# Kernel tuning notes

Hardware: AMD Instinct MI355X
Metric: run time of the kernel (lower is better)

## Reference

```python
import jax, jax.numpy as jnp
import numpy as np

HIDDEN = 512
B, H, W = 8, 48, 48
SCALE = 1.0 / np.sqrt(HIDDEN).astype(np.float32)


def conv1x1(x, w, b):
    # x: [B, C, H, W], w: [O, C], b: [O]  (1x1 Conv2d == channel matmul)
    return jnp.einsum('bchw,oc->bohw', x, w) + b[None, :, None, None]


def setup_inputs() -> dict:
    key = jax.random.key(0)
    ks = jax.random.split(key, 10)
    s = 1.0 / np.sqrt(HIDDEN)
    return {
        'locx': jax.random.normal(ks[0], (B, HIDDEN, H, W), dtype=jnp.float32),
        'glox': jax.random.normal(ks[1], (B, HIDDEN, H, W), dtype=jnp.float32),
        'Wq': jax.random.normal(ks[2], (HIDDEN, HIDDEN), dtype=jnp.float32) * s,
        'bq': jax.random.normal(ks[3], (HIDDEN,), dtype=jnp.float32) * 0.01,
        'Wk': jax.random.normal(ks[4], (HIDDEN, HIDDEN), dtype=jnp.float32) * s,
        'bk': jax.random.normal(ks[5], (HIDDEN,), dtype=jnp.float32) * 0.01,
        'Wv': jax.random.normal(ks[6], (HIDDEN, HIDDEN), dtype=jnp.float32) * s,
        'bv': jax.random.normal(ks[7], (HIDDEN,), dtype=jnp.float32) * 0.01,
        'Wo': jax.random.normal(ks[8], (HIDDEN, HIDDEN), dtype=jnp.float32) * s,
        'bo': jax.random.normal(ks[9], (HIDDEN,), dtype=jnp.float32) * 0.01,
    }


def reference(locx, glox, Wq, bq, Wk, bk, Wv, bv, Wo, bo):
    b, c, h, w = locx.shape
    # 1x1 conv projections
    q = conv1x1(locx, Wq, bq).reshape(b, c, h * w)   # [B, C, N]
    k = conv1x1(glox, Wk, bk).reshape(b, c, -1)      # [B, C, M]
    v = conv1x1(glox, Wv, bv).reshape(b, c, -1)      # [B, C, M]
    # scores = Q^T K / sqrt(hidden)  -> [B, N, M]
    scores = jnp.einsum('bcn,bcm->bnm', q, k) * SCALE
    probs = jax.nn.softmax(scores, axis=-1)           # dropout rate 0.0 -> identity
    # context = probs @ V^T -> [B, N, C] -> [B, C, H, H]
    ctx = jnp.einsum('bnm,bcm->bcn', probs, v).reshape(b, c, h, h)
    out = conv1x1(ctx, Wo, bo)                        # proj dropout 0.0 -> identity
    return out
```

## Files before the change

### kernel.cpp

```cpp
#include <hip/hip_runtime.h>
#include <hip/hip_bf16.h>

typedef __attribute__((ext_vector_type(4))) float f32x4;
typedef __attribute__((ext_vector_type(8))) short bf16x8;
typedef __attribute__((ext_vector_type(4))) short s16x4;

#define C_DIM 512
#define N_PIX 2304
#define N_BATCH 8
#define ATT_SCALE 0.04419417382415922f
#define NJB 9

typedef __attribute__((address_space(3))) unsigned int lds_u32;
typedef const __attribute__((address_space(1))) unsigned int glob_u32;

__device__ __forceinline__ void gl2lds16(const __hip_bfloat16* g, __hip_bfloat16* l)
{
    __builtin_amdgcn_global_load_lds((glob_u32*)g, (lds_u32*)l, 16, 0, 0);
}

#define GBAR() __builtin_amdgcn_s_barrier()
#define GVM0() asm volatile("s_waitcnt vmcnt(0)" ::: "memory")


#define BAR()  __builtin_amdgcn_s_barrier()
#define LGK0() asm volatile("s_waitcnt lgkmcnt(0)" ::: "memory")
#define VM4()  asm volatile("s_waitcnt vmcnt(4)" ::: "memory")
#define VM0()  asm volatile("s_waitcnt vmcnt(0)" ::: "memory")
#define PRIO(p) __builtin_amdgcn_s_setprio(p)

#define STAGE_A(dd, hh, tk) do { \
    _Pragma("unroll") \
    for (int ss = 0; ss < 2; ++ss) { \
        const int ur0 = wave * 16 + ss * 8; \
        const int row0 = ((ur0 >> 6) << 7) + (hh) * 64 + (ur0 & 63); \
        gl2lds16(gA + (size_t)row0 * C_DIM + (tk) * 64, \
                 (__hip_bfloat16*)&LA[dd][row0 * 64]); \
    } } while (0)

#define STAGE_B(dd, bb, tk) do { \
    _Pragma("unroll") \
    for (int ss = 0; ss < 2; ++ss) { \
        const int ur0 = wave * 16 + ss * 8; \
        const int row0 = ((ur0 >> 5) << 6) + (bb) * 32 + (ur0 & 31); \
        gl2lds16(gB + (size_t)row0 * C_DIM + (tk) * 64, \
                 (__hip_bfloat16*)&LB[dd][row0 * 64]); \
    } } while (0)

#define LOAD_A(dd, hh) do { \
    _Pragma("unroll") \
    for (int tt = 0; tt < 4; ++tt) { \
        const int rb = (wr * 128 + (hh) * 64 + tt * 16 + fr) * 64; \
        _Pragma("unroll") \
        for (int kk = 0; kk < 2; ++kk) \
            aF[tt][kk] = *(const bf16x8*)(&LA[dd][rb + (((kk * 4 + fq) ^ sw) << 3)]); \
    } } while (0)

#define LOAD_B(dd, bb, dst) do { \
    _Pragma("unroll") \
    for (int s2 = 0; s2 < 2; ++s2) { \
        const int rb = (wc * 64 + (bb) * 32 + s2 * 16 + fr) * 64; \
        _Pragma("unroll") \
        for (int kk = 0; kk < 2; ++kk) \
            dst[s2][kk] = *(const bf16x8*)(&LB[dd][rb + (((kk * 4 + fq) ^ sw) << 3)]); \
    } } while (0)

#define MFMA_Q(HH, BB, bsrc) do { \
    _Pragma("unroll") \
    for (int tt = 0; tt < 4; ++tt) \
    _Pragma("unroll") \
    for (int s2 = 0; s2 < 2; ++s2) \
    _Pragma("unroll") \
    for (int kk = 0; kk < 2; ++kk) \
        acc[(HH) * 4 + tt][(BB) * 2 + s2] = __builtin_amdgcn_mfma_f32_16x16x32_bf16( \
            aF[tt][kk], bsrc[s2][kk], acc[(HH) * 4 + tt][(BB) * 2 + s2], 0, 0, 0); \
    } while (0)

template<int NS>
__global__ __launch_bounds__(512, 2)
void s_vp(const __hip_bfloat16* __restrict__ Qt, const __hip_bfloat16* __restrict__ Kt,
          __hip_bfloat16* __restrict__ Pu, float* __restrict__ rp,
          const __hip_bfloat16* __restrict__ wo, const __hip_bfloat16* __restrict__ Vt,
          __hip_bfloat16* __restrict__ Vp, int bz_off, long sPu)
{
    __shared__ __hip_bfloat16 LA[2][256 * 64];
    __shared__ __hip_bfloat16 LB[2][256 * 64];

    const int lin = blockIdx.x;
    const int bz  = lin % NS + bz_off;
    const int t   = lin / NS;
    const bool is_s = (t < 81);

    int ib, jb;
    const __hip_bfloat16 *A, *B;
    __hip_bfloat16* D;
    const long sQ = (long)N_PIX * C_DIM;
    if (is_s) {
        ib = t / 9; jb = t % 9;
        A = Qt + (size_t)bz * sQ;
        B = Kt + (size_t)bz * sQ;
        D = Pu + (size_t)bz * (size_t)sPu;
    } else {
        int u = t - 81;
        ib = u / 9; jb = u % 9;
        A = wo;
        B = Vt + (size_t)bz * sQ;
        D = Vp + (size_t)bz * sQ;
    }
    const int i0 = ib * 256;
    const int j0 = jb * 256;

    const int tid  = threadIdx.x;
    const int lane = tid & 63;
    const int wave = tid >> 6;

    const int lrow = lane >> 3;
    const int lcs  = (lane & 7) ^ lrow;
    const __hip_bfloat16* gA = A + (size_t)(i0 + lrow) * C_DIM + lcs * 8;
    const __hip_bfloat16* gB = B + (size_t)(j0 + lrow) * C_DIM + lcs * 8;

    const int fr = lane & 15;
    const int fq = lane >> 4;
    const int sw = fr & 7;
    const int wr = wave >> 2;
    const int wc = wave & 3;

    f32x4 acc[8][4];
#pragma unroll
    for (int a = 0; a < 8; ++a)
#pragma unroll
        for (int b = 0; b < 4; ++b)
            acc[a][b] = (f32x4){0.f, 0.f, 0.f, 0.f};

    bf16x8 aF[4][2], bF0[2][2], bF1[2][2];

    STAGE_A(0, 0, 0); STAGE_B(0, 0, 0); STAGE_B(0, 1, 0); STAGE_A(0, 1, 0);
    STAGE_A(1, 0, 1); STAGE_B(1, 1, 1);
    VM4();
    BAR();

    for (int kt = 0; kt < 6; ++kt) {
        const int d = kt & 1, e = d ^ 1;
        LOAD_A(d, 0); LOAD_B(d, 0, bF0);
        STAGE_A(e, 1, kt + 1);
        BAR(); LGK0();
        PRIO(1); MFMA_Q(0, 0, bF0); PRIO(0);
        BAR();
        LOAD_B(d, 1, bF1);
        STAGE_B(e, 0, kt + 1);
        BAR(); LGK0();
        PRIO(1); MFMA_Q(0, 1, bF1); PRIO(0);
        BAR();
        LOAD_A(d, 1);
        STAGE_A(d, 0, kt + 2);
        BAR(); LGK0();
        PRIO(1); MFMA_Q(1, 1, bF1); PRIO(0);
        BAR();
        STAGE_B(d, 1, kt + 2);
        VM4();
        BAR();
        PRIO(1); MFMA_Q(1, 0, bF0); PRIO(0);
        BAR();
    }
    {
        LOAD_A(0, 0); LOAD_B(0, 0, bF0);
        STAGE_A(1, 1, 7);
        BAR(); LGK0();
        PRIO(1); MFMA_Q(0, 0, bF0); PRIO(0);
        BAR();
        LOAD_B(0, 1, bF1);
        STAGE_B(1, 0, 7);
        BAR(); LGK0();
        PRIO(1); MFMA_Q(0, 1, bF1); PRIO(0);
        BAR();
        LOAD_A(0, 1);
        BAR(); LGK0();
        PRIO(1); MFMA_Q(1, 1, bF1); PRIO(0);
        BAR();
        VM0();
        BAR();
        PRIO(1); MFMA_Q(1, 0, bF0); PRIO(0);
        BAR();
    }
    {
        LOAD_A(1, 0); LOAD_B(1, 0, bF0);
        BAR(); LGK0();
        PRIO(1); MFMA_Q(0, 0, bF0); PRIO(0);
        BAR();
        LOAD_B(1, 1, bF1);
        BAR(); LGK0();
        PRIO(1); MFMA_Q(0, 1, bF1); PRIO(0);
        BAR();
        LOAD_A(1, 1);
        BAR(); LGK0();
        PRIO(1); MFMA_Q(1, 1, bF1); PRIO(0);
        BAR();
        PRIO(1); MFMA_Q(1, 0, bF0); PRIO(0);
    }

    if (is_s) {
        float rpart[8][4];
#pragma unroll
        for (int a = 0; a < 8; ++a)
#pragma unroll
            for (int r = 0; r < 4; ++r)
                rpart[a][r] = 0.f;
#pragma unroll
        for (int a = 0; a < 8; ++a) {
            const int grow = i0 + wr * 128 + a * 16 + fq * 4;
#pragma unroll
            for (int b = 0; b < 4; ++b) {
                const int col = j0 + wc * 64 + b * 16 + fr;
#pragma unroll
                for (int r = 0; r < 4; ++r) {
                    float v = __expf(acc[a][b][r] * ATT_SCALE);
                    rpart[a][r] += v;
                    D[(size_t)(grow + r) * N_PIX + col] = __float2bfloat16(v);
                }
            }
        }
#pragma unroll
        for (int m = 1; m < 16; m <<= 1)
#pragma unroll
            for (int a = 0; a < 8; ++a)
#pragma unroll
                for (int r = 0; r < 4; ++r)
                    rpart[a][r] += __shfl_xor(rpart[a][r], m);
        float* rsl = (float*)&LA[0][0];
        __syncthreads();
        if (fr == 0) {
#pragma unroll
            for (int a = 0; a < 8; ++a)
#pragma unroll
                for (int r = 0; r < 4; ++r)
                    rsl[wave * 128 + a * 16 + fq * 4 + r] = rpart[a][r];
        }
        __syncthreads();
        if (tid < 256) {
            const int wr2 = tid >> 7, rl = tid & 127;
            float s = rsl[(wr2 * 4 + 0) * 128 + rl] + rsl[(wr2 * 4 + 1) * 128 + rl]
                    + rsl[(wr2 * 4 + 2) * 128 + rl] + rsl[(wr2 * 4 + 3) * 128 + rl];
            rp[((size_t)jb * N_BATCH + bz) * N_PIX + i0 + tid] = s;
        }
    } else {
#pragma unroll
        for (int a = 0; a < 8; ++a) {
            const int grow = i0 + wr * 128 + a * 16 + fq * 4;
#pragma unroll
            for (int b = 0; b < 4; ++b) {
                const int col = j0 + wc * 64 + b * 16 + fr;
#pragma unroll
                for (int r = 0; r < 4; ++r)
                    D[(size_t)(grow + r) * N_PIX + col] = __float2bfloat16(acc[a][b][r]);
            }
        }
    }
}

#undef STAGE_A
#undef STAGE_B
#undef LOAD_A
#undef LOAD_B
#undef MFMA_Q
#undef BAR
#undef LGK0
#undef VM4
#undef VM0
#undef PRIO


#define PV_STAGE(ee, tk) do { \
    _Pragma("unroll") \
    for (int ss = 0; ss < 2; ++ss) \
        gl2lds16(ga + (size_t)ss * 8 * N_PIX + (tk) * 64, \
                 laA + (ee) * (64 * 64) + ss * 8 * 64); \
    _Pragma("unroll") \
    for (int ss = 0; ss < 4; ++ss) \
        gl2lds16(gb + (size_t)ss * 8 * N_PIX + (tk) * 64, \
                 laB + (ee) * (128 * 64) + ss * 8 * 64); \
    } while (0)

#define PV_COMP(dd) do { \
    _Pragma("unroll") \
    for (int kk = 0; kk < 2; ++kk) { \
        bf16x8 af[2], bfr[4]; \
        const int ca = ((kk * 4 + fq) ^ sw) << 3; \
        _Pragma("unroll") \
        for (int tt = 0; tt < 2; ++tt) \
            af[tt]  = *(const bf16x8*)(&As[dd][(wi + tt * 16 + fr) * 64 + ca]); \
        _Pragma("unroll") \
        for (int tt = 0; tt < 4; ++tt) \
            bfr[tt] = *(const bf16x8*)(&Bs[dd][(wj + tt * 16 + fr) * 64 + ca]); \
        _Pragma("unroll") \
        for (int a = 0; a < 2; ++a) \
        _Pragma("unroll") \
        for (int b = 0; b < 4; ++b) \
            acc[a][b] = __builtin_amdgcn_mfma_f32_16x16x32_bf16( \
                af[a], bfr[b], acc[a][b], 0, 0, 0); \
    } } while (0)

template<int NS>
__global__ __launch_bounds__(256)
void pv_out(const __hip_bfloat16* __restrict__ Vp, const __hip_bfloat16* __restrict__ Pu,
            float* __restrict__ out, const float* __restrict__ bo,
            const float* __restrict__ rp, int bz_off, long sPu)
{
    __shared__ __hip_bfloat16 As[2][64 * 64];
    __shared__ __hip_bfloat16 Bs[2][128 * 64];

    const int lin = blockIdx.x;
    const int bz  = lin % NS + bz_off;
    const int t   = lin / NS;
    const int ib  = t % 8;
    const int jb  = t / 8;
    const int i0  = ib * 64;
    const int j0  = jb * 128;

    const long sCN = (long)C_DIM * N_PIX;
    const __hip_bfloat16* A = Vp + (size_t)bz * sCN;
    const __hip_bfloat16* B = Pu + (size_t)bz * (size_t)sPu;
    float* D = out + (size_t)bz * sCN;

    const int tid  = threadIdx.x;
    const int lane = tid & 63;
    const int wave = tid >> 6;

    const int lrow = lane >> 3;
    const int lcs  = (lane & 7) ^ lrow;
    const __hip_bfloat16* ga = A + (size_t)(i0 + wave * 16 + lrow) * N_PIX + lcs * 8;
    const __hip_bfloat16* gb = B + (size_t)(j0 + wave * 32 + lrow) * N_PIX + lcs * 8;
    __hip_bfloat16* laA = &As[0][wave * 16 * 64];
    __hip_bfloat16* laB = &Bs[0][wave * 32 * 64];

    const int fr = lane & 15;
    const int fq = lane >> 4;
    const int sw = fr & 7;
    const int wi = (wave >> 1) * 32;
    const int wj = (wave & 1) * 64;

    f32x4 acc[2][4];
#pragma unroll
    for (int a = 0; a < 2; ++a)
#pragma unroll
        for (int b = 0; b < 4; ++b)
            acc[a][b] = (f32x4){0.f, 0.f, 0.f, 0.f};

    PV_STAGE(0, 0);
    GVM0(); GBAR();

#pragma unroll 1
    for (int kt = 0; kt < 34; kt += 2) {
        PV_STAGE(1, kt + 1);
        PV_COMP(0);
        GVM0(); GBAR();
        PV_STAGE(0, kt + 2);
        PV_COMP(1);
        GVM0(); GBAR();
    }
    PV_STAGE(1, 35);
    PV_COMP(0);
    GVM0(); GBAR();
    PV_COMP(1);

    const int orow = fq * 4;
    float rjv[4];
#pragma unroll
    for (int b = 0; b < 4; ++b) {
        int j = j0 + wj + b * 16 + fr;
        float s = 0.f;
#pragma unroll
        for (int jj = 0; jj < NJB; ++jj)
            s += rp[((size_t)jj * N_BATCH + bz) * N_PIX + j];
        rjv[b] = 1.f / s;
    }

#pragma unroll
    for (int a = 0; a < 2; ++a) {
        int ibx = i0 + wi + a * 16 + orow;
#pragma unroll
        for (int r = 0; r < 4; ++r) {
            float bi = bo[ibx + r];
#pragma unroll
            for (int b = 0; b < 4; ++b) {
                int j = j0 + wj + b * 16 + fr;
                D[(size_t)(ibx + r) * N_PIX + j] = acc[a][b][r] * rjv[b] + bi;
            }
        }
    }
}

#undef PV_STAGE
#undef PV_COMP


#define PJ_STAGE(ee, tk) do { \
    _Pragma("unroll") \
    for (int ss = 0; ss < 4; ++ss) { \
        gl2lds16(ga + (size_t)ss * 8 * C_DIM + (tk) * 64, \
                 laA + (ee) * (128 * 64) + ss * 8 * 64); \
        gl2lds16(gb + (size_t)ss * 8 * C_DIM + (tk) * 64, \
                 laB + (ee) * (128 * 64) + ss * 8 * 64); \
    } } while (0)

#define PJ_COMP(dd) do { \
    _Pragma("unroll") \
    for (int kk = 0; kk < 2; ++kk) { \
        bf16x8 af[4], bfr[4]; \
        const int ca = ((kk * 4 + fq) ^ sw) << 3; \
        _Pragma("unroll") \
        for (int tt = 0; tt < 4; ++tt) { \
            af[tt]  = *(const bf16x8*)(&As[dd][(wi + tt * 16 + fr) * 64 + ca]); \
            bfr[tt] = *(const bf16x8*)(&Bs[dd][(wj + tt * 16 + fr) * 64 + ca]); \
        } \
        _Pragma("unroll") \
        for (int a = 0; a < 4; ++a) \
        _Pragma("unroll") \
        for (int b = 0; b < 4; ++b) \
            acc[a][b] = __builtin_amdgcn_mfma_f32_16x16x32_bf16( \
                af[a], bfr[b], acc[a][b], 0, 0, 0); \
    } } while (0)

__global__ __launch_bounds__(256)
void proj_qkv(const __hip_bfloat16* __restrict__ Xl,
              const __hip_bfloat16* __restrict__ Xg,
              const __hip_bfloat16* __restrict__ wgt,
              const float* __restrict__ bq, const float* __restrict__ bk,
              const float* __restrict__ bv,
              __hip_bfloat16* __restrict__ QKV)
{
    __shared__ __hip_bfloat16 As[2][128 * 64];
    __shared__ __hip_bfloat16 Bs[2][128 * 64];

    const int lin = blockIdx.x;
    const int s   = lin % 24;
    const int bz  = s & 7;
    const int mat = s >> 3;
    const int t   = lin / 24;
    const int j0  = (t & 3) * 128;
    const int i0  = (t >> 2) * 128;

    const __hip_bfloat16* Ab = ((mat == 0) ? Xl : Xg) + (size_t)bz * N_PIX * C_DIM;
    const __hip_bfloat16* Bb = wgt + (size_t)mat * C_DIM * C_DIM;
    const float* bias = (mat == 0) ? bq : (mat == 1) ? bk : bv;
    __hip_bfloat16* D = QKV + ((size_t)mat * N_BATCH + bz) * N_PIX * C_DIM;

    const int tid  = threadIdx.x;
    const int lane = tid & 63;
    const int wave = tid >> 6;

    const int lrow = lane >> 3;
    const int lcs  = (lane & 7) ^ lrow;
    const __hip_bfloat16* ga = Ab + (size_t)(i0 + wave * 32 + lrow) * C_DIM + lcs * 8;
    const __hip_bfloat16* gb = Bb + (size_t)(j0 + wave * 32 + lrow) * C_DIM + lcs * 8;
    __hip_bfloat16* laA = &As[0][wave * 32 * 64];
    __hip_bfloat16* laB = &Bs[0][wave * 32 * 64];

    const int fr = lane & 15;
    const int fq = lane >> 4;
    const int sw = fr & 7;
    const int wi = (wave >> 1) * 64;
    const int wj = (wave & 1) * 64;

    f32x4 acc[4][4];
#pragma unroll
    for (int a = 0; a < 4; ++a)
#pragma unroll
        for (int b = 0; b < 4; ++b)
            acc[a][b] = (f32x4){0.f, 0.f, 0.f, 0.f};

    PJ_STAGE(0, 0);
    GVM0(); GBAR();

#pragma unroll 1
    for (int kt = 0; kt < 6; kt += 2) {
        PJ_STAGE(1, kt + 1);
        PJ_COMP(0);
        GVM0(); GBAR();
        PJ_STAGE(0, kt + 2);
        PJ_COMP(1);
        GVM0(); GBAR();
    }
    PJ_STAGE(1, 7);
    PJ_COMP(0);
    GVM0(); GBAR();
    PJ_COMP(1);

    const int orow = fq * 4;
#pragma unroll
    for (int a = 0; a < 4; ++a) {
        int ibx = i0 + wi + a * 16 + orow;
#pragma unroll
        for (int b = 0; b < 4; ++b) {
            int j = j0 + wj + b * 16 + fr;
            float bj = bias[j];
#pragma unroll
            for (int r = 0; r < 4; ++r)
                D[(size_t)(ibx + r) * C_DIM + j] = __float2bfloat16(acc[a][b][r] + bj);
        }
    }
}

#undef PJ_STAGE
#undef PJ_COMP

__global__ __launch_bounds__(256)
void prep(const float* __restrict__ locx, const float* __restrict__ glox,
          __hip_bfloat16* __restrict__ Xl, __hip_bfloat16* __restrict__ Xg,
          const float* __restrict__ w0, const float* __restrict__ w1,
          const float* __restrict__ w2, const float* __restrict__ w3,
          __hip_bfloat16* __restrict__ wgt)
{
    const int lin = blockIdx.x;
    const int tid = threadIdx.x;

    if (lin < 4608) {
        __shared__ float t[64 * 65];
        const int z  = lin & 15;
        const int t2 = lin >> 4;
        const int c0 = (t2 & 7) * 64;
        const int n0 = (t2 >> 3) * 64;
        const size_t b = z & 7;
        const float* Xb = ((z < 8) ? locx : glox) + b * (size_t)C_DIM * N_PIX;
        __hip_bfloat16* Xt = (z < 8) ? Xl : Xg;

        const int n_l = tid & 63;
        const int c_b = tid >> 6;
#pragma unroll
        for (int s = 0; s < 16; ++s) {
            int c_l = c_b + s * 4;
            t[c_l * 65 + n_l] = Xb[(size_t)(c0 + c_l) * N_PIX + n0 + n_l];
        }
        __syncthreads();

        const int cc = (tid & 7) * 8;
        const int nb = tid >> 3;
#pragma unroll
        for (int it = 0; it < 2; ++it) {
            int n2 = nb + it * 32;
            union { __hip_bfloat16 h[8]; int4 v; } u;
#pragma unroll
            for (int w = 0; w < 8; ++w)
                u.h[w] = __float2bfloat16(t[(cc + w) * 65 + n2]);
            *(int4*)(&Xt[(b * N_PIX + n0 + n2) * C_DIM + c0 + cc]) = u.v;
        }
    } else {
        const int idx = lin - 4608;
        const int w   = idx >> 8;
        const float* srcs[4] = {w0, w1, w2, w3};
        const int i = ((idx & 255) * 256 + tid) * 4;
        float4 f = *(const float4*)(srcs[w] + i);
        union { __hip_bfloat16 h[4]; s16x4 q; } u;
        u.h[0] = __float2bfloat16(f.x);
        u.h[1] = __float2bfloat16(f.y);
        u.h[2] = __float2bfloat16(f.z);
        u.h[3] = __float2bfloat16(f.w);
        *(s16x4*)(wgt + (size_t)w * C_DIM * C_DIM + i) = u.q;
    }
}

extern "C" void kernel_launch(void* const* d_in, const int* in_sizes, int n_in,
                              void* d_out, int out_size, void* d_ws, size_t ws_size,
                              hipStream_t stream)
{
    const float* locx = (const float*)d_in[0];
    const float* glox = (const float*)d_in[1];
    const float* Wq = (const float*)d_in[2];
    const float* bq = (const float*)d_in[3];
    const float* Wk = (const float*)d_in[4];
    const float* bk = (const float*)d_in[5];
    const float* Wv = (const float*)d_in[6];
    const float* bv = (const float*)d_in[7];
    const float* Wo = (const float*)d_in[8];
    const float* bo = (const float*)d_in[9];
    float* out = (float*)d_out;

    const int C = C_DIM, N = N_PIX;
    const size_t WB   = (size_t)C * C * 2;
    const size_t szX  = (size_t)N_BATCH * N * C * 2;
    const size_t szP1 = (size_t)N * N * 2;
    const size_t szRP = (size_t)NJB * N_BATCH * N * 4;

    const size_t fixed = 4 * WB + 6 * szX + szRP;
    bool full = (ws_size >= fixed + 8 * szP1 + 4096);

    char* ws = (char*)d_ws;
    size_t off = 0;
    auto alloc = [&](size_t bytes) {
        char* p = ws + off;
        off += (bytes + 255) & ~(size_t)255;
        return p;
    };
    __hip_bfloat16* wgt = (__hip_bfloat16*)alloc(4 * WB);
    __hip_bfloat16* Xl  = (__hip_bfloat16*)alloc(szX);
    __hip_bfloat16* Xg  = (__hip_bfloat16*)alloc(szX);
    __hip_bfloat16* QKV = (__hip_bfloat16*)alloc(3 * szX);
    __hip_bfloat16* Vp  = (__hip_bfloat16*)alloc(szX);
    float*          rp  = (float*)alloc(szRP);
    __hip_bfloat16* Pu  = (__hip_bfloat16*)alloc(full ? 8 * szP1 : szP1);

    __hip_bfloat16* Qt = QKV;
    __hip_bfloat16* Kt = QKV + (size_t)N_BATCH * N * C;
    __hip_bfloat16* Vt = QKV + 2 * (size_t)N_BATCH * N * C;
    __hip_bfloat16* wo_b = wgt + 3 * (size_t)C * C;

    const dim3 blk(256);

    prep<<<dim3(5632), blk, 0, stream>>>(locx, glox, Xl, Xg, Wq, Wk, Wv, Wo, wgt);
    proj_qkv<<<dim3(24 * 72), blk, 0, stream>>>(Xl, Xg, wgt, bq, bk, bv, QKV);

    if (full) {
        s_vp<8><<<dim3(8 * 99), dim3(512), 0, stream>>>(
            Qt, Kt, Pu, rp, wo_b, Vt, Vp, 0, (long)N * N);
        pv_out<8><<<dim3(8 * 144), blk, 0, stream>>>(
            Vp, Pu, out, bo, rp, 0, (long)N * N);
    } else {
        for (int r = 0; r < N_BATCH; ++r) {
            s_vp<1><<<dim3(99), dim3(512), 0, stream>>>(
                Qt, Kt, Pu, rp, wo_b, Vt, Vp, r, 0);
            pv_out<1><<<dim3(144), blk, 0, stream>>>(
                Vp, Pu, out, bo, rp, r, 0);
        }
    }
}
```

Measured before the change: 329.6 us.

## Fold Q/K and V/O weights into combined matrices to drop projection GEMMs

Rewrites the attention algebraically. Scores become Xl·(Wq^T Wk)·Xg^T plus a per-key term Xg·(Wk^T bq); the per-query terms cancel in softmax, which is why bk is dropped. The V and output projections are merged into one Wo·Wv matrix, applied directly to Xg with a folded bias Wo·bv, and written transposed. This removes one full projection GEMM and the separate Wo·V tiles in the score kernel, at the cost of an extra small weight-mixing kernel and more bf16 rounding through the combined weights.

Result: slower. 359.9 us (+9.2%).

```diff
diff --git a/kernel.cpp b/kernel.cpp
--- a/kernel.cpp
+++ b/kernel.cpp
@@ -21,6 +21,7 @@
 
 #define GBAR() __builtin_amdgcn_s_barrier()
 #define GVM0() asm volatile("s_waitcnt vmcnt(0)" ::: "memory")
+
 
 
 #define BAR()  __builtin_amdgcn_s_barrier()
@@ -78,10 +79,9 @@
 
 template<int NS>
 __global__ __launch_bounds__(512, 2)
-void s_vp(const __hip_bfloat16* __restrict__ Qt, const __hip_bfloat16* __restrict__ Kt,
-          __hip_bfloat16* __restrict__ Pu, float* __restrict__ rp,
-          const __hip_bfloat16* __restrict__ wo, const __hip_bfloat16* __restrict__ Vt,
-          __hip_bfloat16* __restrict__ Vp, int bz_off, long sPu)
+void s_only(const __hip_bfloat16* __restrict__ Tm, const __hip_bfloat16* __restrict__ Xgt,
+            __hip_bfloat16* __restrict__ Pu, float* __restrict__ rp,
+            const float* __restrict__ vvec, int bz_off, long sPu)
 {
     __shared__ __hip_bfloat16 LA[2][256 * 64];
     __shared__ __hip_bfloat16 LB[2][256 * 64];
@@ -89,24 +89,14 @@
     const int lin = blockIdx.x;
     const int bz  = lin % NS + bz_off;
     const int t   = lin / NS;
-    const bool is_s = (t < 81);
-
-    int ib, jb;
-    const __hip_bfloat16 *A, *B;
-    __hip_bfloat16* D;
+    const int ib  = t / 9;
+    const int jb  = t % 9;
     const long sQ = (long)N_PIX * C_DIM;
-    if (is_s) {
-        ib = t / 9; jb = t % 9;
-        A = Qt + (size_t)bz * sQ;
-        B = Kt + (size_t)bz * sQ;
-        D = Pu + (size_t)bz * (size_t)sPu;
-    } else {
-        int u = t - 81;
-        ib = u / 9; jb = u % 9;
-        A = wo;
-        B = Vt + (size_t)bz * sQ;
-        D = Vp + (size_t)bz * sQ;
-    }
+
+    const __hip_bfloat16* A = Tm  + (size_t)bz * sQ;
+    const __hip_bfloat16* B = Xgt + (size_t)bz * sQ;
+    __hip_bfloat16* D = Pu + (size_t)bz * (size_t)sPu;
+
     const int i0 = ib * 256;
     const int j0 = jb * 256;
 
@@ -198,62 +188,53 @@
         PRIO(1); MFMA_Q(1, 0, bF0); PRIO(0);
     }
 
-    if (is_s) {
-        float rpart[8][4];
+    float vb[4];
+#pragma unroll
+    for (int b = 0; b < 4; ++b)
+        vb[b] = vvec[(size_t)bz * N_PIX + j0 + wc * 64 + b * 16 + fr];
+
+    float rpart[8][4];
+#pragma unroll
+    for (int a = 0; a < 8; ++a)
+#pragma unroll
+        for (int r = 0; r < 4; ++r)
+            rpart[a][r] = 0.f;
+#pragma unroll
+    for (int a = 0; a < 8; ++a) {
+        const int grow = i0 + wr * 128 + a * 16 + fq * 4;
+#pragma unroll
+        for (int b = 0; b < 4; ++b) {
+            const int col = j0 + wc * 64 + b * 16 + fr;
+#pragma unroll
+            for (int r = 0; r < 4; ++r) {
+                float v = __expf(ATT_SCALE * (acc[a][b][r] + vb[b]));
+                rpart[a][r] += v;
+                D[(size_t)(grow + r) * N_PIX + col] = __float2bfloat16(v);
+            }
+        }
+    }
+#pragma unroll
+    for (int m = 1; m < 16; m <<= 1)
 #pragma unroll
         for (int a = 0; a < 8; ++a)
 #pragma unroll
             for (int r = 0; r < 4; ++r)
-                rpart[a][r] = 0.f;
-#pragma unroll
-        for (int a = 0; a < 8; ++a) {
-            const int grow = i0 + wr * 128 + a * 16 + fq * 4;
-#pragma unroll
-            for (int b = 0; b < 4; ++b) {
-                const int col = j0 + wc * 64 + b * 16 + fr;
-#pragma unroll
-                for (int r = 0; r < 4; ++r) {
-                    float v = __expf(acc[a][b][r] * ATT_SCALE);
-                    rpart[a][r] += v;
-                    D[(size_t)(grow + r) * N_PIX + col] = __float2bfloat16(v);
-                }
-            }
-        }
-#pragma unroll
-        for (int m = 1; m < 16; m <<= 1)
-#pragma unroll
-            for (int a = 0; a < 8; ++a)
-#pragma unroll
-                for (int r = 0; r < 4; ++r)
-                    rpart[a][r] += __shfl_xor(rpart[a][r], m);
-        float* rsl = (float*)&LA[0][0];
-        __syncthreads();
-        if (fr == 0) {
-#pragma unroll
-            for (int a = 0; a < 8; ++a)
-#pragma unroll
-                for (int r = 0; r < 4; ++r)
-                    rsl[wave * 128 + a * 16 + fq * 4 + r] = rpart[a][r];
-        }
-        __syncthreads();
-        if (tid < 256) {
-            const int wr2 = tid >> 7, rl = tid & 127;
-            float s = rsl[(wr2 * 4 + 0) * 128 + rl] + rsl[(wr2 * 4 + 1) * 128 + rl]
-                    + rsl[(wr2 * 4 + 2) * 128 + rl] + rsl[(wr2 * 4 + 3) * 128 + rl];
-            rp[((size_t)jb * N_BATCH + bz) * N_PIX + i0 + tid] = s;
-        }
-    } else {
-#pragma unroll
-        for (int a = 0; a < 8; ++a) {
-            const int grow = i0 + wr * 128 + a * 16 + fq * 4;
-#pragma unroll
-            for (int b = 0; b < 4; ++b) {
-                const int col = j0 + wc * 64 + b * 16 + fr;
-#pragma unroll
-                for (int r = 0; r < 4; ++r)
-                    D[(size_t)(grow + r) * N_PIX + col] = __float2bfloat16(acc[a][b][r]);
-            }
-        }
+                rpart[a][r] += __shfl_xor(rpart[a][r], m);
+    float* rsl = (float*)&LA[0][0];
+    __syncthreads();
+    if (fr == 0) {
+#pragma unroll
+        for (int a = 0; a < 8; ++a)
+#pragma unroll
+            for (int r = 0; r < 4; ++r)
+                rsl[wave * 128 + a * 16 + fq * 4 + r] = rpart[a][r];
+    }
+    __syncthreads();
+    if (tid < 256) {
+        const int wr2 = tid >> 7, rl = tid & 127;
+        float s = rsl[(wr2 * 4 + 0) * 128 + rl] + rsl[(wr2 * 4 + 1) * 128 + rl]
+                + rsl[(wr2 * 4 + 2) * 128 + rl] + rsl[(wr2 * 4 + 3) * 128 + rl];
+        rp[((size_t)jb * N_BATCH + bz) * N_PIX + i0 + tid] = s;
     }
 }
 
@@ -420,29 +401,47 @@
                 af[a], bfr[b], acc[a][b], 0, 0, 0); \
     } } while (0)
 
+#define PJ_LOOP() do { \
+    PJ_STAGE(0, 0); \
+    GVM0(); GBAR(); \
+    _Pragma("unroll 1") \
+    for (int kt = 0; kt < 6; kt += 2) { \
+        PJ_STAGE(1, kt + 1); \
+        PJ_COMP(0); \
+        GVM0(); GBAR(); \
+        PJ_STAGE(0, kt + 2); \
+        PJ_COMP(1); \
+        GVM0(); GBAR(); \
+    } \
+    PJ_STAGE(1, 7); \
+    PJ_COMP(0); \
+    GVM0(); GBAR(); \
+    PJ_COMP(1); \
+    } while (0)
+
 __global__ __launch_bounds__(256)
-void proj_qkv(const __hip_bfloat16* __restrict__ Xl,
-              const __hip_bfloat16* __restrict__ Xg,
-              const __hip_bfloat16* __restrict__ wgt,
-              const float* __restrict__ bq, const float* __restrict__ bk,
-              const float* __restrict__ bv,
-              __hip_bfloat16* __restrict__ QKV)
+void proj2(const __hip_bfloat16* __restrict__ Xlt,
+           const __hip_bfloat16* __restrict__ Xgt,
+           const __hip_bfloat16* __restrict__ matT,
+           const __hip_bfloat16* __restrict__ Wov,
+           const float* __restrict__ bovp,
+           __hip_bfloat16* __restrict__ Tm,
+           __hip_bfloat16* __restrict__ Vp)
 {
     __shared__ __hip_bfloat16 As[2][128 * 64];
     __shared__ __hip_bfloat16 Bs[2][128 * 64];
 
     const int lin = blockIdx.x;
-    const int s   = lin % 24;
+    const int s   = lin % 16;
     const int bz  = s & 7;
-    const int mat = s >> 3;
-    const int t   = lin / 24;
-    const int j0  = (t & 3) * 128;
-    const int i0  = (t >> 2) * 128;
-
-    const __hip_bfloat16* Ab = ((mat == 0) ? Xl : Xg) + (size_t)bz * N_PIX * C_DIM;
-    const __hip_bfloat16* Bb = wgt + (size_t)mat * C_DIM * C_DIM;
-    const float* bias = (mat == 0) ? bq : (mat == 1) ? bk : bv;
-    __hip_bfloat16* D = QKV + ((size_t)mat * N_BATCH + bz) * N_PIX * C_DIM;
+    const int m2  = s >> 3;
+    const int t2  = lin / 16;
+    const int j0  = (t2 & 3) * 128;
+    const int i0  = (t2 >> 2) * 128;
+    const long sNC = (long)N_PIX * C_DIM;
+
+    const __hip_bfloat16* Ab = (m2 ? Xgt : Xlt) + (size_t)bz * sNC;
+    const __hip_bfloat16* Bb = m2 ? Wov : matT;
 
     const int tid  = threadIdx.x;
     const int lane = tid & 63;
@@ -468,22 +467,130 @@
         for (int b = 0; b < 4; ++b)
             acc[a][b] = (f32x4){0.f, 0.f, 0.f, 0.f};
 
-    PJ_STAGE(0, 0);
-    GVM0(); GBAR();
-
-#pragma unroll 1
-    for (int kt = 0; kt < 6; kt += 2) {
-        PJ_STAGE(1, kt + 1);
-        PJ_COMP(0);
-        GVM0(); GBAR();
-        PJ_STAGE(0, kt + 2);
-        PJ_COMP(1);
-        GVM0(); GBAR();
-    }
-    PJ_STAGE(1, 7);
-    PJ_COMP(0);
-    GVM0(); GBAR();
-    PJ_COMP(1);
+    PJ_LOOP();
+
+    const int orow = fq * 4;
+    if (m2 == 0) {
+        __hip_bfloat16* D = Tm + (size_t)bz * sNC;
+#pragma unroll
+        for (int a = 0; a < 4; ++a) {
+            int ibx = i0 + wi + a * 16 + orow;
+#pragma unroll
+            for (int b = 0; b < 4; ++b) {
+                int j = j0 + wj + b * 16 + fr;
+#pragma unroll
+                for (int r = 0; r < 4; ++r)
+                    D[(size_t)(ibx + r) * C_DIM + j] = __float2bfloat16(acc[a][b][r]);
+            }
+        }
+    } else {
+        __hip_bfloat16* Dvp = Vp + (size_t)bz * sNC;
+        float bvb[4];
+#pragma unroll
+        for (int b = 0; b < 4; ++b)
+            bvb[b] = bovp[j0 + wj + b * 16 + fr];
+        __syncthreads();
+        __hip_bfloat16* Tt = (__hip_bfloat16*)&As[0][0];
+#pragma unroll
+        for (int h = 0; h < 2; ++h) {
+            if ((wave & 1) == h) {
+#pragma unroll
+                for (int a = 0; a < 4; ++a) {
+                    int rl = wi + a * 16 + orow;
+#pragma unroll
+                    for (int b = 0; b < 4; ++b) {
+                        int cl = b * 16 + fr;
+#pragma unroll
+                        for (int r = 0; r < 4; ++r)
+                            Tt[(rl + r) * 65 + cl] =
+                                __float2bfloat16(acc[a][b][r] + bvb[b]);
+                    }
+                }
+            }
+            __syncthreads();
+            {
+                const int lj = tid >> 2, ic = (tid & 3) * 32;
+                union { __hip_bfloat16 h8[32]; int4 v4[4]; } u;
+#pragma unroll
+                for (int q = 0; q < 32; ++q)
+                    u.h8[q] = Tt[(ic + q) * 65 + lj];
+                __hip_bfloat16* dst = Dvp + (size_t)(j0 + h * 64 + lj) * N_PIX + i0 + ic;
+#pragma unroll
+                for (int q4 = 0; q4 < 4; ++q4)
+                    ((int4*)dst)[q4] = u.v4[q4];
+            }
+            __syncthreads();
+        }
+    }
+}
+
+__global__ __launch_bounds__(256)
+void wmix(const __hip_bfloat16* __restrict__ WkT, const __hip_bfloat16* __restrict__ WqT,
+          const __hip_bfloat16* __restrict__ wo_bf, const __hip_bfloat16* __restrict__ WvT,
+          __hip_bfloat16* __restrict__ matT, __hip_bfloat16* __restrict__ Wov,
+          const __hip_bfloat16* __restrict__ Xgt, const float* __restrict__ wvbuf,
+          float* __restrict__ vvec)
+{
+    __shared__ __hip_bfloat16 As[2][128 * 64];
+    __shared__ __hip_bfloat16 Bs[2][128 * 64];
+
+    const int lin = blockIdx.x;
+    const int tid = threadIdx.x;
+
+    if (lin >= 32) {
+        float* wvs = (float*)&As[0][0];
+        wvs[tid] = wvbuf[tid];
+        wvs[tid + 256] = wvbuf[tid + 256];
+        __syncthreads();
+        const int blk = lin - 32;
+        const int b   = blk / 9;
+        const int m0  = (blk % 9) * 256;
+        const __hip_bfloat16* row = Xgt + ((size_t)b * N_PIX + m0 + tid) * C_DIM;
+        float acc = 0.f;
+#pragma unroll 4
+        for (int c8 = 0; c8 < 64; ++c8) {
+            union { bf16x8 v; __hip_bfloat16 h[8]; } u;
+            u.v = *(const bf16x8*)(row + c8 * 8);
+#pragma unroll
+            for (int j = 0; j < 8; ++j)
+                acc += __bfloat162float(u.h[j]) * wvs[c8 * 8 + j];
+        }
+        vvec[(size_t)b * N_PIX + m0 + tid] = acc;
+        return;
+    }
+
+    const int m2 = lin >> 4;
+    const int t2 = lin & 15;
+    const int j0 = (t2 & 3) * 128;
+    const int i0 = (t2 >> 2) * 128;
+
+    const __hip_bfloat16* Ab = m2 ? wo_bf : WkT;
+    const __hip_bfloat16* Bb = m2 ? WvT   : WqT;
+    __hip_bfloat16* D = m2 ? Wov : matT;
+
+    const int lane = tid & 63;
+    const int wave = tid >> 6;
+    const int lrow = lane >> 3;
+    const int lcs  = (lane & 7) ^ lrow;
+    const __hip_bfloat16* ga = Ab + (size_t)(i0 + wave * 32 + lrow) * C_DIM + lcs * 8;
+    const __hip_bfloat16* gb = Bb + (size_t)(j0 + wave * 32 + lrow) * C_DIM + lcs * 8;
+    __hip_bfloat16* laA = &As[0][wave * 32 * 64];
+    __hip_bfloat16* laB = &Bs[0][wave * 32 * 64];
+
+    const int fr = lane & 15;
+    const int fq = lane >> 4;
+    const int sw = fr & 7;
+    const int wi = (wave >> 1) * 64;
+    const int wj = (wave & 1) * 64;
+
+    f32x4 acc[4][4];
+#pragma unroll
+    for (int a = 0; a < 4; ++a)
+#pragma unroll
+        for (int b = 0; b < 4; ++b)
+            acc[a][b] = (f32x4){0.f, 0.f, 0.f, 0.f};
+
+    PJ_LOOP();
 
     const int orow = fq * 4;
 #pragma unroll
@@ -492,36 +599,40 @@
 #pragma unroll
         for (int b = 0; b < 4; ++b) {
             int j = j0 + wj + b * 16 + fr;
-            float bj = bias[j];
 #pragma unroll
             for (int r = 0; r < 4; ++r)
-                D[(size_t)(ibx + r) * C_DIM + j] = __float2bfloat16(acc[a][b][r] + bj);
+                D[(size_t)(ibx + r) * C_DIM + j] = __float2bfloat16(acc[a][b][r]);
         }
     }
 }
 
 #undef PJ_STAGE
 #undef PJ_COMP
+#undef PJ_LOOP
 
 __global__ __launch_bounds__(256)
 void prep(const float* __restrict__ locx, const float* __restrict__ glox,
-          __hip_bfloat16* __restrict__ Xl, __hip_bfloat16* __restrict__ Xg,
-          const float* __restrict__ w0, const float* __restrict__ w1,
-          const float* __restrict__ w2, const float* __restrict__ w3,
-          __hip_bfloat16* __restrict__ wgt)
+          __hip_bfloat16* __restrict__ Xlt, __hip_bfloat16* __restrict__ Xgt,
+          const float* __restrict__ Wq, const float* __restrict__ Wk,
+          const float* __restrict__ Wv, const float* __restrict__ Wo,
+          __hip_bfloat16* __restrict__ wo_bf,
+          __hip_bfloat16* __restrict__ WqT, __hip_bfloat16* __restrict__ WkT,
+          __hip_bfloat16* __restrict__ WvT,
+          const float* __restrict__ bq, const float* __restrict__ bv,
+          float* __restrict__ wvbuf, float* __restrict__ bovbuf)
 {
+    __shared__ float t[64 * 65];
     const int lin = blockIdx.x;
     const int tid = threadIdx.x;
 
     if (lin < 4608) {
-        __shared__ float t[64 * 65];
         const int z  = lin & 15;
         const int t2 = lin >> 4;
         const int c0 = (t2 & 7) * 64;
         const int n0 = (t2 >> 3) * 64;
         const size_t b = z & 7;
         const float* Xb = ((z < 8) ? locx : glox) + b * (size_t)C_DIM * N_PIX;
-        __hip_bfloat16* Xt = (z < 8) ? Xl : Xg;
+        __hip_bfloat16* Xt = (z < 8) ? Xlt : Xgt;
 
         const int n_l = tid & 63;
         const int c_b = tid >> 6;
@@ -543,18 +654,66 @@
                 u.h[w] = __float2bfloat16(t[(cc + w) * 65 + n2]);
             *(int4*)(&Xt[(b * N_PIX + n0 + n2) * C_DIM + c0 + cc]) = u.v;
         }
-    } else {
+    } else if (lin < 4864) {
         const int idx = lin - 4608;
-        const int w   = idx >> 8;
-        const float* srcs[4] = {w0, w1, w2, w3};
-        const int i = ((idx & 255) * 256 + tid) * 4;
-        float4 f = *(const float4*)(srcs[w] + i);
+        const int i = (idx * 256 + tid) * 4;
+        float4 f = *(const float4*)(Wo + i);
         union { __hip_bfloat16 h[4]; s16x4 q; } u;
         u.h[0] = __float2bfloat16(f.x);
         u.h[1] = __float2bfloat16(f.y);
         u.h[2] = __float2bfloat16(f.z);
         u.h[3] = __float2bfloat16(f.w);
-        *(s16x4*)(wgt + (size_t)w * C_DIM * C_DIM + i) = u.q;
+        *(s16x4*)(wo_bf + i) = u.q;
+    } else if (lin < 5056) {
+        const int widx = lin - 4864;
+        const int w    = widx >> 6;
+        const int tile = widx & 63;
+        const float* S = (w == 0) ? Wq : (w == 1) ? Wk : Wv;
+        __hip_bfloat16* Dt = (w == 0) ? WqT : (w == 1) ? WkT : WvT;
+        const int o0  = (tile & 7) * 64;
+        const int c0t = (tile >> 3) * 64;
+
+        const int n_l = tid & 63;
+        const int c_b = tid >> 6;
+#pragma unroll
+        for (int s = 0; s < 16; ++s) {
+            int o_l = c_b + s * 4;
+            t[o_l * 65 + n_l] = S[(size_t)(o0 + o_l) * 512 + c0t + n_l];
+        }
+        __syncthreads();
+
+        const int cc = (tid & 7) * 8;
+        const int nb = tid >> 3;
+#pragma unroll
+        for (int it = 0; it < 2; ++it) {
+            int c_r = nb + it * 32;
+            union { __hip_bfloat16 h[8]; int4 v; } u;
+#pragma unroll
+            for (int w8 = 0; w8 < 8; ++w8)
+                u.h[w8] = __float2bfloat16(t[(cc + w8) * 65 + c_r]);
+            *(int4*)(&Dt[(size_t)(c0t + c_r) * 512 + o0 + cc]) = u.v;
+        }
+    } else if (lin == 5056) {
+        float a0 = 0.f, a1 = 0.f;
+        for (int o = 0; o < 512; ++o) {
+            float bb = bq[o];
+            a0 += Wk[(size_t)o * 512 + tid] * bb;
+            a1 += Wk[(size_t)o * 512 + tid + 256] * bb;
+        }
+        wvbuf[tid] = a0;
+        wvbuf[tid + 256] = a1;
+    } else {
+#pragma unroll
+        for (int half = 0; half < 2; ++half) {
+            int o = tid + half * 256;
+            float acc = 0.f;
+            for (int c4 = 0; c4 < 128; ++c4) {
+                float4 f = *(const float4*)(Wo + (size_t)o * 512 + c4 * 4);
+                float4 g = *(const float4*)(bv + c4 * 4);
+                acc += f.x * g.x + f.y * g.y + f.z * g.z + f.w * g.w;
+            }
+            bovbuf[o] = acc;
+        }
     }
 }
 
@@ -573,15 +732,14 @@
     const float* Wo = (const float*)d_in[8];
     const float* bo = (const float*)d_in[9];
     float* out = (float*)d_out;
+    (void)bk;
 
     const int C = C_DIM, N = N_PIX;
     const size_t WB   = (size_t)C * C * 2;
     const size_t szX  = (size_t)N_BATCH * N * C * 2;
     const size_t szP1 = (size_t)N * N * 2;
     const size_t szRP = (size_t)NJB * N_BATCH * N * 4;
-
-    const size_t fixed = 4 * WB + 6 * szX + szRP;
-    bool full = (ws_size >= fixed + 8 * szP1 + 4096);
+    const size_t szV  = (size_t)N_BATCH * N * 4;
 
     char* ws = (char*)d_ws;
     size_t off = 0;
@@ -590,33 +748,42 @@
         off += (bytes + 255) & ~(size_t)255;
         return p;
     };
-    __hip_bfloat16* wgt = (__hip_bfloat16*)alloc(4 * WB);
-    __hip_bfloat16* Xl  = (__hip_bfloat16*)alloc(szX);
-    __hip_bfloat16* Xg  = (__hip_bfloat16*)alloc(szX);
-    __hip_bfloat16* QKV = (__hip_bfloat16*)alloc(3 * szX);
-    __hip_bfloat16* Vp  = (__hip_bfloat16*)alloc(szX);
-    float*          rp  = (float*)alloc(szRP);
-    __hip_bfloat16* Pu  = (__hip_bfloat16*)alloc(full ? 8 * szP1 : szP1);
-
-    __hip_bfloat16* Qt = QKV;
-    __hip_bfloat16* Kt = QKV + (size_t)N_BATCH * N * C;
-    __hip_bfloat16* Vt = QKV + 2 * (size_t)N_BATCH * N * C;
-    __hip_bfloat16* wo_b = wgt + 3 * (size_t)C * C;
+    __hip_bfloat16* wo_bf = (__hip_bfloat16*)alloc(WB);
+    __hip_bfloat16* WqT   = (__hip_bfloat16*)alloc(WB);
+    __hip_bfloat16* WkT   = (__hip_bfloat16*)alloc(WB);
+    __hip_bfloat16* WvT   = (__hip_bfloat16*)alloc(WB);
+    __hip_bfloat16* matT  = (__hip_bfloat16*)alloc(WB);
+    __hip_bfloat16* Wov   = (__hip_bfloat16*)alloc(WB);
+    float*          wvb   = (float*)alloc(512 * 4);
+    float*          bovb  = (float*)alloc(512 * 4);
+    float*          vvec  = (float*)alloc(szV);
+    __hip_bfloat16* Xlt   = (__hip_bfloat16*)alloc(szX);
+    __hip_bfloat16* Xgt   = (__hip_bfloat16*)alloc(szX);
+    __hip_bfloat16* Tm    = (__hip_bfloat16*)alloc(szX);
+    __hip_bfloat16* Vp    = (__hip_bfloat16*)alloc(szX);
+    float*          rp    = (float*)alloc(szRP);
+    const size_t fixed = off;
+    bool full = (ws_size >= fixed + 8 * szP1 + 4096);
+    __hip_bfloat16* Pu = (__hip_bfloat16*)alloc(full ? 8 * szP1 : szP1);
 
     const dim3 blk(256);
 
-    prep<<<dim3(5632), blk, 0, stream>>>(locx, glox, Xl, Xg, Wq, Wk, Wv, Wo, wgt);
-    proj_qkv<<<dim3(24 * 72), blk, 0, stream>>>(Xl, Xg, wgt, bq, bk, bv, QKV);
+    prep<<<dim3(5058), blk, 0, stream>>>(locx, glox, Xlt, Xgt,
+                                         Wq, Wk, Wv, Wo, wo_bf, WqT, WkT, WvT,
+                                         bq, bv, wvb, bovb);
+    wmix<<<dim3(104), blk, 0, stream>>>(WkT, WqT, wo_bf, WvT, matT, Wov,
+                                        Xgt, wvb, vvec);
+    proj2<<<dim3(16 * 72), blk, 0, stream>>>(Xlt, Xgt, matT, Wov, bovb, Tm, Vp);
 
     if (full) {
-        s_vp<8><<<dim3(8 * 99), dim3(512), 0, stream>>>(
-            Qt, Kt, Pu, rp, wo_b, Vt, Vp, 0, (long)N * N);
+        s_only<8><<<dim3(8 * 81), dim3(512), 0, stream>>>(
+            Tm, Xgt, Pu, rp, vvec, 0, (long)N * N);
         pv_out<8><<<dim3(8 * 144), blk, 0, stream>>>(
             Vp, Pu, out, bo, rp, 0, (long)N * N);
     } else {
         for (int r = 0; r < N_BATCH; ++r) {
-            s_vp<1><<<dim3(99), dim3(512), 0, stream>>>(
-                Qt, Kt, Pu, rp, wo_b, Vt, Vp, r, 0);
+            s_only<1><<<dim3(81), dim3(512), 0, stream>>>(
+                Tm, Xgt, Pu, rp, vvec, r, 0);
             pv_out<1><<<dim3(144), blk, 0, stream>>>(
                 Vp, Pu, out, bo, rp, r, 0);
         }
```
